# Kernel tuning notes

Measured on AMD Instinct MI355X. Metric: run time of the kernel, lower is better.

Reference implementation:

```python
import jax, jax.numpy as jnp
import numpy as np

N_NODES, N_LAYERS, D = 4096, 8, 128


def setup_inputs() -> dict:
    key = jax.random.key(0)
    k1, k2, k3 = jax.random.split(key, 3)
    feature = jax.random.normal(k1, (N_NODES, N_LAYERS, D), dtype=jnp.float32)
    W = jax.random.uniform(k2, (D, D), dtype=jnp.float32)
    adj = jax.random.randint(k3, (N_LAYERS, N_NODES, N_NODES), 0, 2, dtype=jnp.int32)
    return {"feature": feature, "W": W, "adj": adj}


def reference(feature, W, adj):
    # feature: [N, L, D]; W: [D, D]; adj: [L, N, N] with 0/1 entries.
    # Original loop: for i, for l, for j in neighbors(i) U {i}:
    #     ret[j, l, :] = (W @ feature[i, l, :]) / sqrt(d_i * d_j)   # OVERWRITE
    # => final ret[j, l] uses the LAST source i with adj[l,i,j]==1 or i==j.
    L, N = adj.shape[0], adj.shape[1]
    i_idx = jnp.arange(N)
    # mask[l, i, j]: source i writes to destination j at layer l
    mask = (adj == 1) | (i_idx[:, None] == i_idx[None, :])
    # last (largest) source index per (l, j); diagonal guarantees >= 0
    src = jnp.max(jnp.where(mask, i_idx[:, None], -1), axis=1)          # [L, N]
    deg = jnp.sum(adj, axis=2).astype(feature.dtype) + 1.0              # [L, N]
    # shared tiny GEMM applied to all (node, layer) features
    Wf = jnp.einsum('de,nle->lnd', W, feature)                          # [L, N, D]
    gathered = jnp.take_along_axis(Wf, src[:, :, None], axis=1)         # [L, N, D]
    d_src = jnp.take_along_axis(deg, src, axis=1)                       # [L, N]
    scale = 1.0 / jnp.sqrt(d_src * deg)                                 # [L, N]
    ret = jnp.transpose(gathered * scale[:, :, None], (1, 0, 2))        # [N, L, D]
    return ret
```

## Files before the change

### kernel.cpp

```cpp
#include <hip/hip_runtime.h>
#include <cstddef>

#define NN 4096
#define NL 8
#define ND 128

#define SRC_BLOCKS (NL * (NN / 256))

typedef int   int4v   __attribute__((ext_vector_type(4)));
typedef float float4v __attribute__((ext_vector_type(4)));

__global__ __launch_bounds__(256) void degsrc_kernel(const int* __restrict__ adj,
                                                     float* __restrict__ deg,
                                                     int* __restrict__ src) {
  if (blockIdx.x < SRC_BLOCKS) {
    const int bid = blockIdx.x;
    const int l = bid >> 4;
    const int j = ((bid & 15) << 8) + threadIdx.x;
    const int* __restrict__ A = adj + (size_t)l * NN * NN + j;
    int cur = j;
    bool found = false;
    int itop = NN - 1;
    while (true) {
      int ibot = itop - 31;
      if (ibot < 0) ibot = 0;
      int best = -1;
#pragma unroll
      for (int k = 0; k < 32; ++k) {
        int i = itop - k;
        int a = (i >= ibot) ? A[(size_t)i * NN] : 0;
        int c = (a != 0 && i > j) ? i : -1;
        if (c > best) best = c;
      }
      if (!found && best >= 0) { cur = best; found = true; }
      bool done = found || (ibot <= j + 1);
      if (__syncthreads_and((int)done)) break;
      itop = ibot - 1;
    }
    src[l * NN + j] = cur;
  } else {
    const size_t row2 = (size_t)(blockIdx.x - SRC_BLOCKS) * 2;
    const int r = threadIdx.x >> 7;
    const int t = threadIdx.x & 127;
    const int4v* __restrict__ p =
        reinterpret_cast<const int4v*>(adj + (row2 + r) * (size_t)NN);
    int s = 0;
#pragma unroll
    for (int k = 0; k < 8; ++k) {
      int4v v = __builtin_nontemporal_load(&p[t + k * 128]);
      s += v.x + v.y + v.z + v.w;
    }
    for (int off = 32; off > 0; off >>= 1) s += __shfl_down(s, off, 64);
    __shared__ int ws[4];
    if ((threadIdx.x & 63) == 0) ws[threadIdx.x >> 6] = s;
    __syncthreads();
    if (threadIdx.x == 0)   deg[row2]     = (float)(ws[0] + ws[1]) + 1.0f;
    if (threadIdx.x == 128) deg[row2 + 1] = (float)(ws[2] + ws[3]) + 1.0f;
  }
}

#define JT 128
__global__ __launch_bounds__(256, 1) void out_kernel(
    const float* __restrict__ feature, const float* __restrict__ W,
    const float* __restrict__ deg, const int* __restrict__ src,
    float* __restrict__ out) {
  __shared__ float Wl[128 * 128];
  __shared__ float fb[JT * 128];

  const int l = blockIdx.y;
  const int jbase = blockIdx.x * JT;

  for (int q = threadIdx.x; q < 128 * 32; q += 256) {
    int dd = q >> 5, eq = q & 31;
    float4v v = reinterpret_cast<const float4v*>(W)[q];
    *reinterpret_cast<float4v*>(&Wl[dd * 128 + 4 * (eq ^ (dd & 7))]) = v;
  }
  for (int q = threadIdx.x; q < JT * 32; q += 256) {
    int jj = q >> 5, eq = q & 31;
    int s = src[l * NN + jbase + jj];
    float4v v = reinterpret_cast<const float4v*>(
        feature + ((size_t)s * NL + l) * ND)[eq];
    *reinterpret_cast<float4v*>(&fb[jj * 128 + 4 * (eq ^ ((jj >> 3) & 7))]) = v;
  }
  __syncthreads();

  const int u = threadIdx.x & 15;
  const int g = threadIdx.x >> 4;
  const int wsw = u & 7;
  const int fsw = g & 7;

  float acc[8][8];
#pragma unroll
  for (int dd = 0; dd < 8; ++dd)
#pragma unroll
    for (int jj = 0; jj < 8; ++jj) acc[dd][jj] = 0.0f;

#pragma unroll 2
  for (int eq = 0; eq < 32; ++eq) {
    float4v w[8], f[8];
#pragma unroll
    for (int dd = 0; dd < 8; ++dd)
      w[dd] = *reinterpret_cast<const float4v*>(
          &Wl[(u + dd * 16) * 128 + 4 * (eq ^ wsw)]);
#pragma unroll
    for (int jj = 0; jj < 8; ++jj)
      f[jj] = *reinterpret_cast<const float4v*>(
          &fb[(g * 8 + jj) * 128 + 4 * (eq ^ fsw)]);
#pragma unroll
    for (int dd = 0; dd < 8; ++dd)
#pragma unroll
      for (int jj = 0; jj < 8; ++jj)
        acc[dd][jj] += w[dd].x * f[jj].x + w[dd].y * f[jj].y +
                       w[dd].z * f[jj].z + w[dd].w * f[jj].w;
  }

#pragma unroll
  for (int jj = 0; jj < 8; ++jj) {
    const int j = jbase + g * 8 + jj;
    const int s = src[l * NN + j];
    const float scj = rsqrtf(deg[l * NN + s] * deg[l * NN + j]);
    float* o = out + ((size_t)j * NL + l) * ND;
#pragma unroll
    for (int dd = 0; dd < 8; ++dd) o[u + dd * 16] = acc[dd][jj] * scj;
  }
}

extern "C" void kernel_launch(void* const* d_in, const int* in_sizes, int n_in,
                              void* d_out, int out_size, void* d_ws,
                              size_t ws_size, hipStream_t stream) {
  const float* feature = (const float*)d_in[0];
  const float* W       = (const float*)d_in[1];
  const int*   adj     = (const int*)d_in[2];
  float* out = (float*)d_out;

  float* deg = (float*)d_ws;
  int*   src = (int*)((char*)d_ws + (size_t)NL * NN * sizeof(float));

  degsrc_kernel<<<SRC_BLOCKS + NL * NN / 2, 256, 0, stream>>>(adj, deg, src);
  out_kernel<<<dim3(NN / JT, NL), 256, 0, stream>>>(feature, W, deg, src, out);
}
```

Baseline: 113.1 us.

## Compute W·feature only for used source nodes, then gather-scale in separate kernel

Records in a bitmask which source nodes are actually selected per layer while computing src, then computes W·feature only for those nodes into a workspace buffer, and finally gathers and scales rows in a lightweight elementwise kernel. Since sources are mostly the last few indices for random dense adjacency, most GEMV work is skipped instead of recomputing a full tiled GEMM per destination. The cost is an extra launch, a workspace round trip for Wf, and a naive per-node GEMV reading W from global memory.

```diff
diff --git a/kernel.cpp b/kernel.cpp
--- a/kernel.cpp
+++ b/kernel.cpp
@@ -10,14 +10,21 @@
 typedef int   int4v   __attribute__((ext_vector_type(4)));
 typedef float float4v __attribute__((ext_vector_type(4)));
 
+
 __global__ __launch_bounds__(256) void degsrc_kernel(const int* __restrict__ adj,
                                                      float* __restrict__ deg,
-                                                     int* __restrict__ src) {
+                                                     int* __restrict__ src,
+                                                     unsigned* __restrict__ used) {
+  __shared__ unsigned lmask[128];
+  __shared__ int ws[4];
+
   if (blockIdx.x < SRC_BLOCKS) {
     const int bid = blockIdx.x;
     const int l = bid >> 4;
     const int j = ((bid & 15) << 8) + threadIdx.x;
     const int* __restrict__ A = adj + (size_t)l * NN * NN + j;
+    if (threadIdx.x < 128) lmask[threadIdx.x] = 0u;
+    __syncthreads();
     int cur = j;
     bool found = false;
     int itop = NN - 1;
@@ -38,6 +45,9 @@
       itop = ibot - 1;
     }
     src[l * NN + j] = cur;
+    atomicOr(&lmask[cur >> 5], 1u << (cur & 31));
+    __syncthreads();
+    if (threadIdx.x < 128) used[bid * 128 + threadIdx.x] = lmask[threadIdx.x];
   } else {
     const size_t row2 = (size_t)(blockIdx.x - SRC_BLOCKS) * 2;
     const int r = threadIdx.x >> 7;
@@ -51,7 +61,6 @@
       s += v.x + v.y + v.z + v.w;
     }
     for (int off = 32; off > 0; off >>= 1) s += __shfl_down(s, off, 64);
-    __shared__ int ws[4];
     if ((threadIdx.x & 63) == 0) ws[threadIdx.x >> 6] = s;
     __syncthreads();
     if (threadIdx.x == 0)   deg[row2]     = (float)(ws[0] + ws[1]) + 1.0f;
@@ -59,70 +68,50 @@
   }
 }
 
-#define JT 128
-__global__ __launch_bounds__(256, 1) void out_kernel(
-    const float* __restrict__ feature, const float* __restrict__ W,
-    const float* __restrict__ deg, const int* __restrict__ src,
-    float* __restrict__ out) {
-  __shared__ float Wl[128 * 128];
-  __shared__ float fb[JT * 128];
+__global__ __launch_bounds__(128) void wf_kernel(const float* __restrict__ feature,
+                                                 const float* __restrict__ W,
+                                                 const unsigned* __restrict__ used,
+                                                 float* __restrict__ Wf) {
+  const int i = blockIdx.x;
+  const int l = blockIdx.y;
+  const int w = i >> 5;
+  const unsigned bit = 1u << (i & 31);
+  unsigned m = 0;
+#pragma unroll
+  for (int c = 0; c < 16; ++c) m |= used[(l * 16 + c) * 128 + w];
+  if (!(m & bit)) return;
 
-  const int l = blockIdx.y;
-  const int jbase = blockIdx.x * JT;
-
-  for (int q = threadIdx.x; q < 128 * 32; q += 256) {
-    int dd = q >> 5, eq = q & 31;
-    float4v v = reinterpret_cast<const float4v*>(W)[q];
-    *reinterpret_cast<float4v*>(&Wl[dd * 128 + 4 * (eq ^ (dd & 7))]) = v;
-  }
-  for (int q = threadIdx.x; q < JT * 32; q += 256) {
-    int jj = q >> 5, eq = q & 31;
-    int s = src[l * NN + jbase + jj];
-    float4v v = reinterpret_cast<const float4v*>(
-        feature + ((size_t)s * NL + l) * ND)[eq];
-    *reinterpret_cast<float4v*>(&fb[jj * 128 + 4 * (eq ^ ((jj >> 3) & 7))]) = v;
-  }
+  __shared__ float fbuf[ND];
+  if (threadIdx.x < 32)
+    reinterpret_cast<float4v*>(fbuf)[threadIdx.x] =
+        reinterpret_cast<const float4v*>(feature + ((size_t)i * NL + l) * ND)[threadIdx.x];
   __syncthreads();
 
-  const int u = threadIdx.x & 15;
-  const int g = threadIdx.x >> 4;
-  const int wsw = u & 7;
-  const int fsw = g & 7;
+  const int d = threadIdx.x;
+  float acc = 0.0f;
+#pragma unroll 8
+  for (int eq = 0; eq < 32; ++eq) {
+    float4v wv = reinterpret_cast<const float4v*>(W + (size_t)d * ND)[eq];
+    float4v fv = reinterpret_cast<const float4v*>(fbuf)[eq];
+    acc += wv.x * fv.x + wv.y * fv.y + wv.z * fv.z + wv.w * fv.w;
+  }
+  Wf[((size_t)l * NN + i) * ND + d] = acc;
+}
 
-  float acc[8][8];
-#pragma unroll
-  for (int dd = 0; dd < 8; ++dd)
-#pragma unroll
-    for (int jj = 0; jj < 8; ++jj) acc[dd][jj] = 0.0f;
-
-#pragma unroll 2
-  for (int eq = 0; eq < 32; ++eq) {
-    float4v w[8], f[8];
-#pragma unroll
-    for (int dd = 0; dd < 8; ++dd)
-      w[dd] = *reinterpret_cast<const float4v*>(
-          &Wl[(u + dd * 16) * 128 + 4 * (eq ^ wsw)]);
-#pragma unroll
-    for (int jj = 0; jj < 8; ++jj)
-      f[jj] = *reinterpret_cast<const float4v*>(
-          &fb[(g * 8 + jj) * 128 + 4 * (eq ^ fsw)]);
-#pragma unroll
-    for (int dd = 0; dd < 8; ++dd)
-#pragma unroll
-      for (int jj = 0; jj < 8; ++jj)
-        acc[dd][jj] += w[dd].x * f[jj].x + w[dd].y * f[jj].y +
-                       w[dd].z * f[jj].z + w[dd].w * f[jj].w;
-  }
-
-#pragma unroll
-  for (int jj = 0; jj < 8; ++jj) {
-    const int j = jbase + g * 8 + jj;
-    const int s = src[l * NN + j];
-    const float scj = rsqrtf(deg[l * NN + s] * deg[l * NN + j]);
-    float* o = out + ((size_t)j * NL + l) * ND;
-#pragma unroll
-    for (int dd = 0; dd < 8; ++dd) o[u + dd * 16] = acc[dd][jj] * scj;
-  }
+__global__ __launch_bounds__(256) void out_kernel(const float* __restrict__ Wf,
+                                                  const float* __restrict__ deg,
+                                                  const int* __restrict__ src,
+                                                  float* __restrict__ out) {
+  const int g = blockIdx.x * 256 + threadIdx.x;
+  const int q = g & 31;
+  const int jl = g >> 5;
+  const int l = jl & 7;
+  const int j = jl >> 3;
+  const int s = src[l * NN + j];
+  const float sc = rsqrtf(deg[l * NN + s] * deg[l * NN + j]);
+  float4v v = reinterpret_cast<const float4v*>(Wf + ((size_t)l * NN + s) * ND)[q];
+  v.x *= sc; v.y *= sc; v.z *= sc; v.w *= sc;
+  __builtin_nontemporal_store(v, reinterpret_cast<float4v*>(out) + g);
 }
 
 extern "C" void kernel_launch(void* const* d_in, const int* in_sizes, int n_in,
@@ -133,9 +122,13 @@
   const int*   adj     = (const int*)d_in[2];
   float* out = (float*)d_out;
 
-  float* deg = (float*)d_ws;
-  int*   src = (int*)((char*)d_ws + (size_t)NL * NN * sizeof(float));
+  char* ws = (char*)d_ws;
+  float*    deg  = (float*)(ws);
+  int*      src  = (int*)(ws + 131072);
+  unsigned* used = (unsigned*)(ws + 262144);
+  float*    Wf   = (float*)(ws + 327680);
 
-  degsrc_kernel<<<SRC_BLOCKS + NL * NN / 2, 256, 0, stream>>>(adj, deg, src);
-  out_kernel<<<dim3(NN / JT, NL), 256, 0, stream>>>(feature, W, deg, src, out);
+  degsrc_kernel<<<SRC_BLOCKS + NL * NN / 2, 256, 0, stream>>>(adj, deg, src, used);
+  wf_kernel<<<dim3(NN, NL), 128, 0, stream>>>(feature, W, used, Wf);
+  out_kernel<<<NN * NL * ND / 4 / 256, 256, 0, stream>>>(Wf, deg, src, out);
 }
```

Result: faster. 108.4 us (-4.2%).
